# Kernel optimization log

Hardware: AMD Instinct MI355X
Metric: run time of the kernel (lower is better)

The kernel has to match this reference:

```python
import jax, jax.numpy as jnp
import numpy as np

B, N, E, G, V = 32, 128, 2048, 1024, 10000
D_IN, HID, MID = 20, 1024, 128
EPS = 1e-5


def _bn(x, gamma, beta, axis):
    # train-mode BatchNorm: biased variance over `axis`
    mu = jnp.mean(x, axis=axis, keepdims=True)
    var = jnp.mean((x - mu) ** 2, axis=axis, keepdims=True)
    return gamma * (x - mu) / jnp.sqrt(var + EPS) + beta


def _gin_mean(h, src, dst):
    # DGL GINConv(apply_func=None, 'mean', eps=0): h + mean over in-neighbors
    b, n, d = h.shape
    offs = (jnp.arange(b, dtype=src.dtype) * n)[:, None]
    sf = (src + offs).reshape(-1)
    df = (dst + offs).reshape(-1)
    hf = h.reshape(b * n, d)
    agg = jax.ops.segment_sum(hf[sf], df, num_segments=b * n)
    deg = jax.ops.segment_sum(jnp.ones(sf.shape, h.dtype), df, num_segments=b * n)
    mean = agg / jnp.maximum(deg, 1.0)[:, None]
    return h + mean.reshape(b, n, d)


def setup_inputs() -> dict:
    key = jax.random.key(0)
    ks = jax.random.split(key, 12)
    inp = {
        'h': jax.random.normal(ks[0], (B, N, D_IN), jnp.float32),
        'edge_src': jax.random.randint(ks[1], (B, E), 0, N),
        'edge_dst': jax.random.randint(ks[2], (B, E), 0, N),
        'gPos': jax.random.randint(ks[3], (B, G), 0, V),
        'allDBGEmb': jax.random.normal(ks[4], (V, HID), jnp.float32) * 0.1,
        'W_init': jax.random.normal(ks[5], (D_IN, HID), jnp.float32) / np.sqrt(D_IN),
        'b_init': jnp.zeros((HID,), jnp.float32),
        'gamma1': jnp.ones((HID,), jnp.float32),
        'beta1': jnp.zeros((HID,), jnp.float32),
        'gamma2': jnp.ones((HID,), jnp.float32),
        'beta2': jnp.zeros((HID,), jnp.float32),
        'W_fc': jax.random.normal(ks[6], (2 * HID, MID), jnp.float32) / np.sqrt(2 * HID),
        'b_fc': jnp.zeros((MID,), jnp.float32),
        'gamma_bn': jnp.ones((MID,), jnp.float32),
        'beta_bn': jnp.zeros((MID,), jnp.float32),
        'W_fc2': jax.random.normal(ks[7], (MID, 1), jnp.float32) / np.sqrt(MID),
        'b_fc2': jnp.zeros((1,), jnp.float32),
    }
    return inp


def reference(h, edge_src, edge_dst, gPos, allDBGEmb, W_init, b_init,
              gamma1, beta1, gamma2, beta2, W_fc, b_fc, gamma_bn, beta_bn,
              W_fc2, b_fc2):
    # per-query-graph GNN encoder
    h2 = h @ W_init + b_init                       # [B,N,HID]
    h2 = jax.nn.relu(_bn(_gin_mean(h2, edge_src, edge_dst), gamma1, beta1, axis=1))
    h2 = jax.nn.relu(_bn(_gin_mean(h2, edge_src, edge_dst), gamma2, beta2, axis=1))
    qemb = jnp.mean(h2, axis=1)                    # [B,HID] (dgl.mean_nodes)
    # pairwise scoring head
    gEmb = allDBGEmb[gPos]                         # [B,G,HID]
    q_rep = jnp.broadcast_to(qemb[:, None, :], gEmb.shape)
    H = jnp.concatenate([q_rep, gEmb], axis=-1)    # [B,G,2*HID]
    H2 = jax.nn.relu(_bn(H @ W_fc + b_fc, gamma_bn, beta_bn, axis=1))  # BN over G
    probs = jax.nn.sigmoid(H2 @ W_fc2 + b_fc2)[..., 0]  # [B,G]
    return probs
```

## Files before the change

### kernel.cpp

```cpp
#include <hip/hip_runtime.h>
#include <hip/hip_bf16.h>

#define BB 32
#define GG 1024
#define VV 10000
#define KHID 1024
#define MM 128
#define NCHUNK 625
#define GEMM_GRID 256

typedef __attribute__((ext_vector_type(8))) short short8;
typedef __attribute__((ext_vector_type(4))) float f32x4;

__device__ __forceinline__ unsigned int pk2(float lo, float hi) {
    __hip_bfloat162 h = __float22bfloat162_rn(make_float2(lo, hi));
    union { __hip_bfloat162 h; unsigned int u; } cv; cv.h = h;
    return cv.u;
}

__device__ __forceinline__ float bfu(unsigned short u) {
    union { unsigned int u; float f; } v; v.u = (unsigned int)u << 16;
    return v.f;
}

__device__ __forceinline__ void lds_barrier() {
    asm volatile("s_waitcnt lgkmcnt(0)" ::: "memory");
    __builtin_amdgcn_s_barrier();
    asm volatile("" ::: "memory");
}

__global__ __launch_bounds__(512, 2) void k_gemm(const float* __restrict__ A,
                                                 const float* __restrict__ Wfc,
                                                 unsigned short* __restrict__ T) {
    const int tid = threadIdx.x;
    const int w = tid >> 6, lane = tid & 63;
    const int r16 = lane & 15, g = lane >> 4;
    const int kbase = w * 128;

    int chunk = blockIdx.x;

    float4 a[8];
    {
        const float* Ap = A + (size_t)(chunk * 16 + r16) * KHID + kbase + g * 8;
#pragma unroll
        for (int kt = 0; kt < 4; ++kt) {
            a[2 * kt]     = *(const float4*)(Ap + kt * 32);
            a[2 * kt + 1] = *(const float4*)(Ap + kt * 32 + 4);
        }
    }

    const float* Wg = Wfc + (size_t)KHID * MM;
    short8 breg[4][8];
#pragma unroll
    for (int kt = 0; kt < 4; ++kt)
#pragma unroll
        for (int t = 0; t < 8; ++t) {
            const float* wp = Wg + (size_t)(kbase + kt * 32 + g * 8) * MM + t * 16 + r16;
            unsigned int* bu = (unsigned int*)&breg[kt][t];
            bu[0] = pk2(wp[0 * MM], wp[1 * MM]);
            bu[1] = pk2(wp[2 * MM], wp[3 * MM]);
            bu[2] = pk2(wp[4 * MM], wp[5 * MM]);
            bu[3] = pk2(wp[6 * MM], wp[7 * MM]);
        }

    __shared__ float red[8][16][128];

    const int orow = tid >> 5, c4 = (tid & 31) * 4;

    while (chunk < NCHUNK) {
        const int next = chunk + GEMM_GRID;

        f32x4 acc[8];
#pragma unroll
        for (int t = 0; t < 8; ++t) acc[t] = (f32x4){0.f, 0.f, 0.f, 0.f};
#pragma unroll
        for (int kt = 0; kt < 4; ++kt) {
            short8 af;
            unsigned int* au = (unsigned int*)&af;
            au[0] = pk2(a[2 * kt].x, a[2 * kt].y);
            au[1] = pk2(a[2 * kt].z, a[2 * kt].w);
            au[2] = pk2(a[2 * kt + 1].x, a[2 * kt + 1].y);
            au[3] = pk2(a[2 * kt + 1].z, a[2 * kt + 1].w);
#pragma unroll
            for (int t = 0; t < 8; ++t)
                acc[t] = __builtin_amdgcn_mfma_f32_16x16x32_bf16(af, breg[kt][t], acc[t],
                                                                 0, 0, 0);
        }

        if (next < NCHUNK) {
            const float* Ap = A + (size_t)(next * 16 + r16) * KHID + kbase + g * 8;
#pragma unroll
            for (int kt = 0; kt < 4; ++kt) {
                a[2 * kt]     = *(const float4*)(Ap + kt * 32);
                a[2 * kt + 1] = *(const float4*)(Ap + kt * 32 + 4);
            }
        }

#pragma unroll
        for (int t = 0; t < 8; ++t)
#pragma unroll
            for (int r = 0; r < 4; ++r)
                red[w][g * 4 + r][t * 16 + r16] = acc[t][r];
        lds_barrier();

        float4 s = *(const float4*)&red[0][orow][c4];
#pragma unroll
        for (int sl = 1; sl < 8; ++sl) {
            float4 p = *(const float4*)&red[sl][orow][c4];
            s.x += p.x; s.y += p.y; s.z += p.z; s.w += p.w;
        }
        *(uint2*)&T[(size_t)(chunk * 16 + orow) * MM + c4] =
            make_uint2(pk2(s.x, s.y), pk2(s.z, s.w));
        lds_barrier();

        chunk = next;
    }
}

__global__ __launch_bounds__(256) void k_stats(const unsigned short* __restrict__ T,
                                               const int* __restrict__ gPos,
                                               float* __restrict__ ps1,
                                               float* __restrict__ ps2) {
    const int b = blockIdx.y, c = blockIdx.x;
    const int tid = threadIdx.x;

    __shared__ int posl[32];
    __shared__ float r1[4][128], r2[4][128];

    if (tid < 32) posl[tid] = gPos[b * GG + c * 32 + tid];
    __syncthreads();

    const int m = tid & 63, q = tid >> 6;
    unsigned int uu[8];
#pragma unroll
    for (int i = 0; i < 8; ++i)
        uu[i] = *(const unsigned int*)&T[(size_t)posl[q * 8 + i] * MM + m * 2];

    float s1a = 0.f, s1b = 0.f, s2a = 0.f, s2b = 0.f;
#pragma unroll
    for (int i = 0; i < 8; ++i) {
        float t0 = bfu((unsigned short)(uu[i] & 0xFFFFu));
        float t1 = bfu((unsigned short)(uu[i] >> 16));
        s1a += t0; s2a += t0 * t0;
        s1b += t1; s2b += t1 * t1;
    }
    r1[q][m * 2] = s1a; r1[q][m * 2 + 1] = s1b;
    r2[q][m * 2] = s2a; r2[q][m * 2 + 1] = s2b;
    __syncthreads();
    if (tid < 128) {
        ps1[((size_t)b * 32 + c) * MM + tid] = r1[0][tid] + r1[1][tid] + r1[2][tid] + r1[3][tid];
        ps2[((size_t)b * 32 + c) * MM + tid] = r2[0][tid] + r2[1][tid] + r2[2][tid] + r2[3][tid];
    }
}

__global__ __launch_bounds__(256) void k_final(const unsigned short* __restrict__ T,
                                               const int* __restrict__ gPos,
                                               const float* __restrict__ ps1,
                                               const float* __restrict__ ps2,
                                               const float* __restrict__ gamma,
                                               const float* __restrict__ beta,
                                               const float* __restrict__ W2,
                                               const float* __restrict__ b2,
                                               float* __restrict__ out) {
    const int b = blockIdx.y, gc = blockIdx.x;
    const int tid = threadIdx.x;

    __shared__ float ssc[128], ssh[128];
    __shared__ int posl[32];
    if (tid < 32) posl[tid] = gPos[b * GG + gc * 32 + tid];
    if (tid >= 128) {
        int mcol = tid - 128;
        float S1 = 0.f, S2 = 0.f;
#pragma unroll
        for (int cc = 0; cc < 32; ++cc) {
            S1 += ps1[((size_t)b * 32 + cc) * MM + mcol];
            S2 += ps2[((size_t)b * 32 + cc) * MM + mcol];
        }
        float mean = S1 * (1.f / 1024.f);
        float var  = S2 * (1.f / 1024.f) - mean * mean;
        float rstd = rsqrtf(var + 1e-5f);
        float sc = gamma[mcol] * rstd;
        ssc[mcol] = sc;
        ssh[mcol] = beta[mcol] - sc * mean;
    }
    __syncthreads();

    const int wave = tid >> 6, lane = tid & 63;
    const int m0 = lane * 2, m1 = lane * 2 + 1;
    const float sc0 = ssc[m0], sh0 = ssh[m0], w20 = W2[m0];
    const float sc1 = ssc[m1], sh1 = ssh[m1], w21 = W2[m1];
    const float bias = b2[0];

    unsigned int uu[8];
#pragma unroll
    for (int i = 0; i < 8; ++i)
        uu[i] = *(const unsigned int*)&T[(size_t)posl[wave * 8 + i] * MM + m0];

#pragma unroll
    for (int i = 0; i < 8; ++i) {
        float t0 = bfu((unsigned short)(uu[i] & 0xFFFFu));
        float t1 = bfu((unsigned short)(uu[i] >> 16));
        float val = fmaxf(sc0 * t0 + sh0, 0.f) * w20 + fmaxf(sc1 * t1 + sh1, 0.f) * w21;
#pragma unroll
        for (int off = 32; off; off >>= 1) val += __shfl_xor(val, off, 64);
        if (lane == 0)
            out[b * GG + gc * 32 + wave * 8 + i] = 1.f / (1.f + __expf(-(val + bias)));
    }
}

extern "C" void kernel_launch(void* const* d_in, const int* in_sizes, int n_in,
                              void* d_out, int out_size, void* d_ws, size_t ws_size,
                              hipStream_t stream) {
    const int*   gPos  = (const int*)d_in[3];
    const float* A     = (const float*)d_in[4];
    const float* Wfc   = (const float*)d_in[11];
    const float* gamma = (const float*)d_in[13];
    const float* beta  = (const float*)d_in[14];
    const float* W2    = (const float*)d_in[15];
    const float* b2    = (const float*)d_in[16];
    float* out = (float*)d_out;

    char* ws = (char*)d_ws;
    unsigned short* T = (unsigned short*)ws;
    float* ps1 = (float*)(ws + (4 << 20));
    float* ps2 = (float*)(ws + (8 << 20));

    hipLaunchKernelGGL(k_gemm, dim3(GEMM_GRID), dim3(512), 0, stream, A, Wfc, T);
    hipLaunchKernelGGL(k_stats, dim3(32, BB), dim3(256), 0, stream, T, gPos, ps1, ps2);
    hipLaunchKernelGGL(k_final, dim3(32, BB), dim3(256), 0, stream, T, gPos, ps1, ps2,
                       gamma, beta, W2, b2, out);
}
```

Measured before the change: 34.08 us.

## Split GEMM K dimension across 16 waves with 1024-thread blocks

The embedding-table GEMM block grows from 8 to 16 waves, so each wave covers 64 K values instead of 128. This halves per-thread register use for the B fragments and A prefetch, and doubles the waves in flight for latency hiding. The trade-off is a 16-way LDS cross-wave reduction instead of 8-way, twice the shared memory (128 KB), and narrower stores to T.

```diff
diff --git a/kernel.cpp b/kernel.cpp
--- a/kernel.cpp
+++ b/kernel.cpp
@@ -29,30 +29,29 @@
     asm volatile("" ::: "memory");
 }
 
-__global__ __launch_bounds__(512, 2) void k_gemm(const float* __restrict__ A,
-                                                 const float* __restrict__ Wfc,
-                                                 unsigned short* __restrict__ T) {
+__global__ __launch_bounds__(1024) void k_gemm(const float* __restrict__ A,
+                                               const float* __restrict__ Wfc,
+                                               unsigned short* __restrict__ T) {
     const int tid = threadIdx.x;
     const int w = tid >> 6, lane = tid & 63;
     const int r16 = lane & 15, g = lane >> 4;
-    const int kbase = w * 128;
+    const int kbase = w * 64;
 
     int chunk = blockIdx.x;
 
-    float4 a[8];
+    float4 a0, a1, a2, a3;
     {
         const float* Ap = A + (size_t)(chunk * 16 + r16) * KHID + kbase + g * 8;
-#pragma unroll
-        for (int kt = 0; kt < 4; ++kt) {
-            a[2 * kt]     = *(const float4*)(Ap + kt * 32);
-            a[2 * kt + 1] = *(const float4*)(Ap + kt * 32 + 4);
-        }
+        a0 = *(const float4*)(Ap);
+        a1 = *(const float4*)(Ap + 4);
+        a2 = *(const float4*)(Ap + 32);
+        a3 = *(const float4*)(Ap + 36);
     }
 
     const float* Wg = Wfc + (size_t)KHID * MM;
-    short8 breg[4][8];
-#pragma unroll
-    for (int kt = 0; kt < 4; ++kt)
+    short8 breg[2][8];
+#pragma unroll
+    for (int kt = 0; kt < 2; ++kt)
 #pragma unroll
         for (int t = 0; t < 8; ++t) {
             const float* wp = Wg + (size_t)(kbase + kt * 32 + g * 8) * MM + t * 16 + r16;
@@ -62,38 +61,48 @@
             bu[2] = pk2(wp[4 * MM], wp[5 * MM]);
             bu[3] = pk2(wp[6 * MM], wp[7 * MM]);
         }
-
-    __shared__ float red[8][16][128];
-
-    const int orow = tid >> 5, c4 = (tid & 31) * 4;
+#pragma unroll
+    for (int kt = 0; kt < 2; ++kt)
+#pragma unroll
+        for (int t = 0; t < 8; ++t)
+            asm volatile("" : "+v"(breg[kt][t]));
+
+    __shared__ float red[16][16][128];
+    const int orow = tid >> 6, c2 = (tid & 63) * 2;
 
     while (chunk < NCHUNK) {
         const int next = chunk + GEMM_GRID;
 
+        short8 af0, af1;
+        {
+            unsigned int* u = (unsigned int*)&af0;
+            u[0] = pk2(a0.x, a0.y); u[1] = pk2(a0.z, a0.w);
+            u[2] = pk2(a1.x, a1.y); u[3] = pk2(a1.z, a1.w);
+        }
+        {
+            unsigned int* u = (unsigned int*)&af1;
+            u[0] = pk2(a2.x, a2.y); u[1] = pk2(a2.z, a2.w);
+            u[2] = pk2(a3.x, a3.y); u[3] = pk2(a3.z, a3.w);
+        }
+
         f32x4 acc[8];
 #pragma unroll
         for (int t = 0; t < 8; ++t) acc[t] = (f32x4){0.f, 0.f, 0.f, 0.f};
 #pragma unroll
-        for (int kt = 0; kt < 4; ++kt) {
-            short8 af;
-            unsigned int* au = (unsigned int*)&af;
-            au[0] = pk2(a[2 * kt].x, a[2 * kt].y);
-            au[1] = pk2(a[2 * kt].z, a[2 * kt].w);
-            au[2] = pk2(a[2 * kt + 1].x, a[2 * kt + 1].y);
-            au[3] = pk2(a[2 * kt + 1].z, a[2 * kt + 1].w);
-#pragma unroll
-            for (int t = 0; t < 8; ++t)
-                acc[t] = __builtin_amdgcn_mfma_f32_16x16x32_bf16(af, breg[kt][t], acc[t],
-                                                                 0, 0, 0);
-        }
+        for (int t = 0; t < 8; ++t)
+            acc[t] = __builtin_amdgcn_mfma_f32_16x16x32_bf16(af0, breg[0][t], acc[t],
+                                                             0, 0, 0);
+#pragma unroll
+        for (int t = 0; t < 8; ++t)
+            acc[t] = __builtin_amdgcn_mfma_f32_16x16x32_bf16(af1, breg[1][t], acc[t],
+                                                             0, 0, 0);
 
         if (next < NCHUNK) {
             const float* Ap = A + (size_t)(next * 16 + r16) * KHID + kbase + g * 8;
-#pragma unroll
-            for (int kt = 0; kt < 4; ++kt) {
-                a[2 * kt]     = *(const float4*)(Ap + kt * 32);
-                a[2 * kt + 1] = *(const float4*)(Ap + kt * 32 + 4);
-            }
+            a0 = *(const float4*)(Ap);
+            a1 = *(const float4*)(Ap + 4);
+            a2 = *(const float4*)(Ap + 32);
+            a3 = *(const float4*)(Ap + 36);
         }
 
 #pragma unroll
@@ -103,14 +112,13 @@
                 red[w][g * 4 + r][t * 16 + r16] = acc[t][r];
         lds_barrier();
 
-        float4 s = *(const float4*)&red[0][orow][c4];
-#pragma unroll
-        for (int sl = 1; sl < 8; ++sl) {
-            float4 p = *(const float4*)&red[sl][orow][c4];
-            s.x += p.x; s.y += p.y; s.z += p.z; s.w += p.w;
-        }
-        *(uint2*)&T[(size_t)(chunk * 16 + orow) * MM + c4] =
-            make_uint2(pk2(s.x, s.y), pk2(s.z, s.w));
+        float sx = 0.f, sy = 0.f;
+#pragma unroll
+        for (int sl = 0; sl < 16; ++sl) {
+            float2 p = *(const float2*)&red[sl][orow][c2];
+            sx += p.x; sy += p.y;
+        }
+        *(unsigned int*)&T[(size_t)(chunk * 16 + orow) * MM + c2] = pk2(sx, sy);
         lds_barrier();
 
         chunk = next;
@@ -225,7 +233,7 @@
     float* ps1 = (float*)(ws + (4 << 20));
     float* ps2 = (float*)(ws + (8 << 20));
 
-    hipLaunchKernelGGL(k_gemm, dim3(GEMM_GRID), dim3(512), 0, stream, A, Wfc, T);
+    hipLaunchKernelGGL(k_gemm, dim3(GEMM_GRID), dim3(1024), 0, stream, A, Wfc, T);
     hipLaunchKernelGGL(k_stats, dim3(32, BB), dim3(256), 0, stream, T, gPos, ps1, ps2);
     hipLaunchKernelGGL(k_final, dim3(32, BB), dim3(256), 0, stream, T, gPos, ps1, ps2,
                        gamma, beta, W2, b2, out);
```

Measured after the change: 38.04 us. 11.6% more time.
